# Optimization experiments

Measured on AMD Instinct MI355X. Metric: run time of the kernel, lower is better.

## Reference

```python
import jax, jax.numpy as jnp
import numpy as np

B, LQ, LK, H = 16, 8192, 128, 128  # note LK == H is required by the final matmul
SCALE = float(np.sqrt(H))


def setup_inputs() -> dict:
    key = jax.random.key(0)
    k1, k2, k3, k4, k5, k6 = jax.random.split(key, 6)
    x1 = jax.random.normal(k1, (B, LQ, H), dtype=jnp.float32)
    x2 = jax.random.normal(k2, (B, LK, H), dtype=jnp.float32)
    x3 = jax.random.randint(k3, (B, LQ, LK), 0, 2).astype(bool)
    bound = 1.0 / np.sqrt(H)  # torch Linear default init
    wq = jax.random.uniform(k4, (H, H), minval=-bound, maxval=bound, dtype=jnp.float32)
    wk = jax.random.uniform(k5, (H, H), minval=-bound, maxval=bound, dtype=jnp.float32)
    wv = jax.random.uniform(k6, (H, H), minval=-bound, maxval=bound, dtype=jnp.float32)
    return {"x1": x1, "x2": x2, "x3": x3, "wq": wq, "wk": wk, "wv": wv}


def reference(x1, x2, x3, wq, wk, wv):
    q = x1 @ wq.T                                   # (B, Lq, H)
    k = x2 @ wk.T                                   # (B, Lk, H)
    qk = jnp.einsum('bqh,bkh->bqk', q, k) / SCALE   # (B, Lq, Lk)
    qk = jnp.where(x3, -jnp.inf, qk)                # masked_fill_ where mask is True
    attn_weight = jax.nn.softmax(qk, axis=-1)       # softmax over Lk
    v = x2 @ wv.T                                   # (B, Lk, H)
    # v @ attn_weight^T: contracts v's H axis with attn_weight's Lk axis (H == Lk)
    attn = jnp.matmul(v, jnp.swapaxes(attn_weight, -2, -1))  # (B, Lk, Lq)
    return attn
```

## Files before the change

### kernel.cpp

```cpp
#include <hip/hip_runtime.h>
#include <hip/hip_bf16.h>
#include <stdint.h>

typedef __bf16 bf16_t;
typedef __bf16 bf16x8 __attribute__((ext_vector_type(8)));
typedef float  f32x4  __attribute__((ext_vector_type(4)));
typedef float  f32x16 __attribute__((ext_vector_type(16)));
typedef unsigned int uint;
typedef uint uintx4 __attribute__((ext_vector_type(4)));

#define MFMA16(a,b,c) __builtin_amdgcn_mfma_f32_16x16x32_bf16((a),(b),(c),0,0,0)
#define MFMA32(a,b,c) __builtin_amdgcn_mfma_f32_32x32x16_bf16((a),(b),(c),0,0,0)

constexpr int NB = 16;
constexpr int LQ = 8192;
constexpr int LK = 128;
constexpr int H  = 128;

constexpr float C1 = 1.4426950408889634f / 11.313708498984761f;

constexpr size_t WS_FLAG = 0;
constexpr size_t WS_MV   = 1024;

__device__ __forceinline__ unsigned swz(unsigned row, unsigned byte) {
  return row * 256u + (byte ^ ((row & 15u) << 4));
}

__device__ __forceinline__ bf16x8 cvt_frag(const float* p) {
  f32x4 u0 = *(const f32x4*)p;
  f32x4 u1 = *(const f32x4*)(p + 4);
  bf16x8 v;
  #pragma unroll
  for (int e = 0; e < 4; ++e) { v[e] = (bf16_t)u0[e]; v[e + 4] = (bf16_t)u1[e]; }
  return v;
}

__device__ __forceinline__ f32x16 zero16() {
  f32x16 z;
  #pragma unroll
  for (int i = 0; i < 16; ++i) z[i] = 0.f;
  return z;
}

__device__ __forceinline__ uint pkbf(float a, float b) {
  uint d;
  asm("v_cvt_pk_bf16_f32 %0, %1, %2" : "=v"(d) : "v"(a), "v"(b));
  return d;
}

__global__ __launch_bounds__(512) void prep_kernel(
    const float* __restrict__ x2, const float* __restrict__ wq,
    const float* __restrict__ wk, const float* __restrict__ wv,
    const unsigned* __restrict__ x3w, uint8_t* __restrict__ ws)
{
  __shared__ uint8_t sP[131072];
  __shared__ int sF32, sBig;
  const int tid = threadIdx.x;
  const int b = blockIdx.x >> 1, which = blockIdx.x & 1;
  const int l = tid & 63, w = tid >> 6, q31 = l & 31, hi2 = l >> 5;
  uint8_t* sOut = sP + 98304;

  if (which == 0) {
    if (blockIdx.x == 0) {
      if (tid == 0) { sF32 = 0; sBig = 0; }
      __syncthreads();
      int f = 0, g = 0;
      #pragma unroll
      for (int j = 0; j < 4; ++j) {
        unsigned v = x3w[tid * 4 + j];
        if (v == 0x3f800000u) f = 1;
        else if (v > 1u) g = 1;
      }
      if (f) sF32 = 1;
      if (g) sBig = 1;
      __syncthreads();
      if (tid == 0) *(int*)(ws + WS_FLAG) = (sF32 == 0 && sBig == 1) ? 1 : 0;
    }

    {
      const int row = tid >> 2, c0 = (tid & 3) * 32;
      #pragma unroll
      for (int wh = 0; wh < 2; ++wh) {
        const float* W = wh ? wk : wq;
        uint8_t* dst = sP + wh * 32768;
        const float* s = W + row * H + c0;
        #pragma unroll
        for (int j = 0; j < 32; ++j)
          *(bf16_t*)(dst + swz(c0 + j, row * 2)) = (bf16_t)s[j];
      }
    }
    __syncthreads();

    {
      const int lo = l & 15, hi = l >> 4;
      bf16x8 a4[4];
      #pragma unroll
      for (int kk = 0; kk < 4; ++kk)
        a4[kk] = *(const bf16x8*)(sP + swz(16 * w + lo, kk * 64 + hi * 16));
      bf16_t* W2T = (bf16_t*)(sP + 65536);
      #pragma unroll
      for (int t = 0; t < 8; ++t) {
        f32x4 c = {0.f, 0.f, 0.f, 0.f};
        #pragma unroll
        for (int kk = 0; kk < 4; ++kk)
          c = MFMA16(a4[kk], *(const bf16x8*)(sP + 32768 + swz(16 * t + lo, kk * 64 + hi * 16)), c);
        #pragma unroll
        for (int r = 0; r < 4; ++r)
          W2T[(16 * w + hi * 4 + r) * H + 16 * t + lo] = (bf16_t)c[r];
      }
    }
    __syncthreads();

    if (w < 4) {
      const int wb = w;
      bf16x8 axf[8];
      const float* x2r = x2 + ((size_t)b * LK + 32 * wb + q31) * H;
      #pragma unroll
      for (int kt = 0; kt < 8; ++kt)
        axf[kt] = cvt_frag(x2r + kt * 16 + 8 * hi2);
      const bf16_t* W2Tl = (const bf16_t*)(sP + 65536);
      #pragma unroll
      for (int nt = 0; nt < 4; ++nt) {
        f32x16 c = zero16();
        #pragma unroll
        for (int kt = 0; kt < 8; ++kt)
          c = MFMA32(axf[kt],
                     *(const bf16x8*)(W2Tl + (size_t)(nt * 32 + q31) * H + kt * 16 + 8 * hi2), c);
        #pragma unroll
        for (int r = 0; r < 16; ++r)
          *(bf16_t*)(sOut + swz(32 * wb + (r & 3) + 8 * (r >> 2) + 4 * hi2,
                                (nt * 32 + q31) * 2)) = (bf16_t)c[r];
      }
    }
  } else {
    if (w < 4) {
      const int wb = w;
      bf16x8 axf[8];
      const float* x2r = x2 + ((size_t)b * LK + 32 * wb + q31) * H;
      #pragma unroll
      for (int kt = 0; kt < 8; ++kt)
        axf[kt] = cvt_frag(x2r + kt * 16 + 8 * hi2);
      #pragma unroll
      for (int nt = 0; nt < 4; ++nt) {
        f32x16 c = zero16();
        #pragma unroll
        for (int kt = 0; kt < 8; ++kt)
          c = MFMA32(axf[kt],
                     cvt_frag(wv + (size_t)(nt * 32 + q31) * H + kt * 16 + 8 * hi2), c);
        #pragma unroll
        for (int r = 0; r < 16; ++r)
          *(bf16_t*)(sOut + swz(32 * wb + (r & 3) + 8 * (r >> 2) + 4 * hi2,
                                (nt * 32 + q31) * 2)) = (bf16_t)c[r];
      }
    }
  }
  __syncthreads();

  {
    const uint4* src = (const uint4*)sOut;
    uint4* dst = (uint4*)(ws + WS_MV + (size_t)b * 65536 + (size_t)which * 32768);
    #pragma unroll
    for (int j = 0; j < 4; ++j)
      dst[tid + j * 512] = src[tid + j * 512];
  }
}

__global__ __launch_bounds__(512, 4) void attn_kernel(
    const float* __restrict__ x1, const void* __restrict__ x3,
    const uint8_t* __restrict__ ws, float* __restrict__ out)
{
  __shared__ uint8_t sm[65536];
  uint8_t* sM = sm;
  uint8_t* sV = sm + 32768;

  const int tid = threadIdx.x, blk = blockIdx.x;
  const int b = blk >> 5, qc = (blk & 31) * 256;
  const int l = tid & 63, w = tid >> 6;
  const int q31 = l & 31, hi2 = l >> 5;
  const int byteMode = *(const int*)(ws + WS_FLAG);

  const int q0w = qc + w * 32;
  const size_t qrow = (size_t)b * LQ + q0w + q31;

  uint4 cp[8];
  {
    const uint4* mvsrc = (const uint4*)(ws + WS_MV + (size_t)b * 65536);
    #pragma unroll
    for (int j = 0; j < 8; ++j)
      cp[j] = mvsrc[tid + j * 512];
  }

  bf16x8 xbf[8];
  {
    const float* xr = x1 + qrow * H;
    #pragma unroll
    for (int kt = 0; kt < 8; ++kt)
      xbf[kt] = cvt_frag(xr + kt * 16 + 8 * hi2);
  }

  uint mu[16];
  if (byteMode) {
    const uint8_t* mp = (const uint8_t*)x3 + qrow * LK;
    #pragma unroll
    for (int jt = 0; jt < 4; ++jt)
      #pragma unroll
      for (int rg = 0; rg < 4; ++rg)
        mu[jt * 4 + rg] = *(const uint*)(mp + jt * 32 + 8 * rg + 4 * hi2);
  }

  {
    uint4* ldst = (uint4*)sm;
    #pragma unroll
    for (int j = 0; j < 8; ++j)
      ldst[tid + j * 512] = cp[j];
  }
  __syncthreads();

  const uint* mrowW = (const uint*)x3 + qrow * LK;
  bf16x8 pb[8];

  #pragma unroll
  for (int half = 0; half < 2; ++half) {
    const int jt0 = half * 2, jt1 = half * 2 + 1;
    f32x16 s0 = zero16(), s1 = zero16();
    #pragma unroll
    for (int kt = 0; kt < 8; ++kt) {
      s0 = MFMA32(*(const bf16x8*)(sM + swz(jt0 * 32 + q31, kt * 32 + hi2 * 16)),
                  xbf[kt], s0);
      s1 = MFMA32(*(const bf16x8*)(sM + swz(jt1 * 32 + q31, kt * 32 + hi2 * 16)),
                  xbf[kt], s1);
    }

    #pragma unroll
    for (int jj = 0; jj < 2; ++jj) {
      f32x16& sj = jj ? s1 : s0;
      const int jt = half * 2 + jj;
      #pragma unroll
      for (int rg = 0; rg < 4; ++rg) {
        uint m0, m1, m2, m3;
        if (byteMode) {
          uint u = mu[jt * 4 + rg];
          m0 = u & 0xffu; m1 = (u >> 8) & 0xffu; m2 = (u >> 16) & 0xffu; m3 = u >> 24;
        } else {
          uint4 mw = *(const uint4*)(mrowW + jt * 32 + 8 * rg + 4 * hi2);
          m0 = mw.x; m1 = mw.y; m2 = mw.z; m3 = mw.w;
        }
        float p0 = __builtin_amdgcn_exp2f(sj[rg * 4 + 0] * C1);
        float p1 = __builtin_amdgcn_exp2f(sj[rg * 4 + 1] * C1);
        float p2 = __builtin_amdgcn_exp2f(sj[rg * 4 + 2] * C1);
        float p3 = __builtin_amdgcn_exp2f(sj[rg * 4 + 3] * C1);
        sj[rg * 4 + 0] = m0 ? 0.f : p0;
        sj[rg * 4 + 1] = m1 ? 0.f : p1;
        sj[rg * 4 + 2] = m2 ? 0.f : p2;
        sj[rg * 4 + 3] = m3 ? 0.f : p3;
      }

      #pragma unroll
      for (int h = 0; h < 2; ++h) {
        uint A = pkbf(sj[h * 8 + 0], sj[h * 8 + 1]);
        uint C = pkbf(sj[h * 8 + 2], sj[h * 8 + 3]);
        uint B = pkbf(sj[h * 8 + 4], sj[h * 8 + 5]);
        uint D = pkbf(sj[h * 8 + 6], sj[h * 8 + 7]);
        asm("v_permlane32_swap_b32 %0, %1" : "+v"(A), "+v"(B));
        asm("v_permlane32_swap_b32 %0, %1" : "+v"(C), "+v"(D));
        uintx4 t; t.x = A; t.y = C; t.z = B; t.w = D;
        pb[jt * 2 + h] = __builtin_bit_cast(bf16x8, t);
      }
    }
  }

  bf16x8 ones1;
  #pragma unroll
  for (int e = 0; e < 8; ++e) ones1[e] = (bf16_t)1.f;

  f32x16 dacc = zero16();
  {
    f32x16 o0 = zero16(), o1 = zero16();
    #pragma unroll
    for (int kt = 0; kt < 8; ++kt) {
      dacc = MFMA32(ones1, pb[kt], dacc);
      o0 = MFMA32(*(const bf16x8*)(sV + swz(0 * 32 + q31, kt * 32 + hi2 * 16)), pb[kt], o0);
      o1 = MFMA32(*(const bf16x8*)(sV + swz(1 * 32 + q31, kt * 32 + hi2 * 16)), pb[kt], o1);
    }
    const float inv = 1.0f / dacc[0];
    #pragma unroll
    for (int r = 0; r < 16; ++r) {
      const int ibase = (r & 3) + 8 * (r >> 2) + 4 * hi2;
      out[((size_t)b * LK + ibase) * LQ + q0w + q31] = o0[r] * inv;
      out[((size_t)b * LK + 32 + ibase) * LQ + q0w + q31] = o1[r] * inv;
    }
  }

  {
    const float inv = 1.0f / dacc[0];
    f32x16 o2 = zero16(), o3 = zero16();
    #pragma unroll
    for (int kt = 0; kt < 8; ++kt) {
      o2 = MFMA32(*(const bf16x8*)(sV + swz(2 * 32 + q31, kt * 32 + hi2 * 16)), pb[kt], o2);
      o3 = MFMA32(*(const bf16x8*)(sV + swz(3 * 32 + q31, kt * 32 + hi2 * 16)), pb[kt], o3);
    }
    #pragma unroll
    for (int r = 0; r < 16; ++r) {
      const int ibase = (r & 3) + 8 * (r >> 2) + 4 * hi2;
      out[((size_t)b * LK + 64 + ibase) * LQ + q0w + q31] = o2[r] * inv;
      out[((size_t)b * LK + 96 + ibase) * LQ + q0w + q31] = o3[r] * inv;
    }
  }
}

extern "C" void kernel_launch(void* const* d_in, const int* in_sizes, int n_in,
                              void* d_out, int out_size, void* d_ws, size_t ws_size,
                              hipStream_t stream) {
  const float* x1 = (const float*)d_in[0];
  const float* x2 = (const float*)d_in[1];
  const void*  x3 = d_in[2];
  const float* wq = (const float*)d_in[3];
  const float* wk = (const float*)d_in[4];
  const float* wv = (const float*)d_in[5];
  uint8_t* ws = (uint8_t*)d_ws;
  float* out = (float*)d_out;

  prep_kernel<<<2 * NB, 512, 0, stream>>>(x2, wq, wk, wv, (const unsigned*)x3, ws);
  attn_kernel<<<NB * (LQ / 256), 512, 0, stream>>>(x1, x3, ws, out);
}
```

Baseline: 49.75 us.

## Process two query tiles per wave with prefetch overlap and async LDS loads

Result: faster. 47.40 us (-4.7%).

```diff
diff --git a/kernel.cpp b/kernel.cpp
--- a/kernel.cpp
+++ b/kernel.cpp
@@ -46,6 +46,12 @@
   uint d;
   asm("v_cvt_pk_bf16_f32 %0, %1, %2" : "=v"(d) : "v"(a), "v"(b));
   return d;
+}
+
+__device__ __forceinline__ void gl16(const void* g, void* l) {
+  __builtin_amdgcn_global_load_lds(
+      (const __attribute__((address_space(1))) uint32_t*)g,
+      (__attribute__((address_space(3))) uint32_t*)l, 16, 0, 0);
 }
 
 __global__ __launch_bounds__(512) void prep_kernel(
@@ -165,7 +171,113 @@
   }
 }
 
-__global__ __launch_bounds__(512, 4) void attn_kernel(
+
+#define CONV_S_PB(XR, MU, QROW)                                                \
+  {                                                                            \
+    bf16x8 xbf[8];                                                             \
+    _Pragma("unroll")                                                          \
+    for (int kt = 0; kt < 8; ++kt) {                                           \
+      _Pragma("unroll")                                                        \
+      for (int e = 0; e < 4; ++e) {                                            \
+        xbf[kt][e]     = (bf16_t)XR[2 * kt][e];                                \
+        xbf[kt][e + 4] = (bf16_t)XR[2 * kt + 1][e];                            \
+      }                                                                        \
+    }                                                                          \
+    const uint* mrowW = (const uint*)x3 + (QROW) * LK;                         \
+    _Pragma("unroll")                                                          \
+    for (int half = 0; half < 2; ++half) {                                     \
+      const int jt0 = half * 2, jt1 = half * 2 + 1;                            \
+      f32x16 s0 = zero16(), s1 = zero16();                                     \
+      __builtin_amdgcn_s_setprio(1);                                           \
+      _Pragma("unroll")                                                        \
+      for (int kt = 0; kt < 8; ++kt) {                                         \
+        s0 = MFMA32(*(const bf16x8*)(sM + swz(jt0 * 32 + q31, kt * 32 + hi2 * 16)), \
+                    xbf[kt], s0);                                              \
+        s1 = MFMA32(*(const bf16x8*)(sM + swz(jt1 * 32 + q31, kt * 32 + hi2 * 16)), \
+                    xbf[kt], s1);                                              \
+      }                                                                        \
+      __builtin_amdgcn_s_setprio(0);                                           \
+      _Pragma("unroll")                                                        \
+      for (int jj = 0; jj < 2; ++jj) {                                         \
+        f32x16& sj = jj ? s1 : s0;                                             \
+        const int jt = half * 2 + jj;                                          \
+        _Pragma("unroll")                                                      \
+        for (int rg = 0; rg < 4; ++rg) {                                       \
+          uint m0, m1, m2, m3;                                                 \
+          if (byteMode) {                                                      \
+            uint u = MU[jt * 4 + rg];                                          \
+            m0 = u & 0xffu; m1 = (u >> 8) & 0xffu;                             \
+            m2 = (u >> 16) & 0xffu; m3 = u >> 24;                              \
+          } else {                                                             \
+            uint4 mw = *(const uint4*)(mrowW + jt * 32 + 8 * rg + 4 * hi2);    \
+            m0 = mw.x; m1 = mw.y; m2 = mw.z; m3 = mw.w;                        \
+          }                                                                    \
+          float p0 = __builtin_amdgcn_exp2f(sj[rg * 4 + 0] * C1);              \
+          float p1 = __builtin_amdgcn_exp2f(sj[rg * 4 + 1] * C1);              \
+          float p2 = __builtin_amdgcn_exp2f(sj[rg * 4 + 2] * C1);              \
+          float p3 = __builtin_amdgcn_exp2f(sj[rg * 4 + 3] * C1);              \
+          sj[rg * 4 + 0] = m0 ? 0.f : p0;                                      \
+          sj[rg * 4 + 1] = m1 ? 0.f : p1;                                      \
+          sj[rg * 4 + 2] = m2 ? 0.f : p2;                                      \
+          sj[rg * 4 + 3] = m3 ? 0.f : p3;                                      \
+        }                                                                      \
+        _Pragma("unroll")                                                      \
+        for (int h = 0; h < 2; ++h) {                                          \
+          uint A = pkbf(sj[h * 8 + 0], sj[h * 8 + 1]);                         \
+          uint C = pkbf(sj[h * 8 + 2], sj[h * 8 + 3]);                         \
+          uint B = pkbf(sj[h * 8 + 4], sj[h * 8 + 5]);                         \
+          uint D = pkbf(sj[h * 8 + 6], sj[h * 8 + 7]);                         \
+          asm("v_permlane32_swap_b32 %0, %1" : "+v"(A), "+v"(B));              \
+          asm("v_permlane32_swap_b32 %0, %1" : "+v"(C), "+v"(D));              \
+          uintx4 t2; t2.x = A; t2.y = C; t2.z = B; t2.w = D;                   \
+          pb[jt * 2 + h] = __builtin_bit_cast(bf16x8, t2);                     \
+        }                                                                      \
+      }                                                                        \
+    }                                                                          \
+  }
+
+#define O_STORE(Q0W)                                                           \
+  {                                                                            \
+    f32x16 dacc = zero16();                                                    \
+    {                                                                          \
+      f32x16 o0 = zero16(), o1 = zero16();                                     \
+      __builtin_amdgcn_s_setprio(1);                                           \
+      _Pragma("unroll")                                                        \
+      for (int kt = 0; kt < 8; ++kt) {                                         \
+        dacc = MFMA32(ones1, pb[kt], dacc);                                    \
+        o0 = MFMA32(*(const bf16x8*)(sV + swz(0 * 32 + q31, kt * 32 + hi2 * 16)), pb[kt], o0); \
+        o1 = MFMA32(*(const bf16x8*)(sV + swz(1 * 32 + q31, kt * 32 + hi2 * 16)), pb[kt], o1); \
+      }                                                                        \
+      __builtin_amdgcn_s_setprio(0);                                           \
+      const float inv = 1.0f / dacc[0];                                        \
+      _Pragma("unroll")                                                        \
+      for (int r = 0; r < 16; ++r) {                                           \
+        const int ibase = (r & 3) + 8 * (r >> 2) + 4 * hi2;                    \
+        __builtin_nontemporal_store(o0[r] * inv,                               \
+            &out[((size_t)b * LK + ibase) * LQ + (Q0W) + q31]);                \
+        __builtin_nontemporal_store(o1[r] * inv,                               \
+            &out[((size_t)b * LK + 32 + ibase) * LQ + (Q0W) + q31]);           \
+      }                                                                        \
+      f32x16 o2 = zero16(), o3 = zero16();                                     \
+      __builtin_amdgcn_s_setprio(1);                                           \
+      _Pragma("unroll")                                                        \
+      for (int kt = 0; kt < 8; ++kt) {                                         \
+        o2 = MFMA32(*(const bf16x8*)(sV + swz(2 * 32 + q31, kt * 32 + hi2 * 16)), pb[kt], o2); \
+        o3 = MFMA32(*(const bf16x8*)(sV + swz(3 * 32 + q31, kt * 32 + hi2 * 16)), pb[kt], o3); \
+      }                                                                        \
+      __builtin_amdgcn_s_setprio(0);                                           \
+      _Pragma("unroll")                                                        \
+      for (int r = 0; r < 16; ++r) {                                           \
+        const int ibase = (r & 3) + 8 * (r >> 2) + 4 * hi2;                    \
+        __builtin_nontemporal_store(o2[r] * inv,                               \
+            &out[((size_t)b * LK + 64 + ibase) * LQ + (Q0W) + q31]);           \
+        __builtin_nontemporal_store(o3[r] * inv,                               \
+            &out[((size_t)b * LK + 96 + ibase) * LQ + (Q0W) + q31]);           \
+      }                                                                        \
+    }                                                                          \
+  }
+
+__global__ __launch_bounds__(256, 2) void attn_kernel(
     const float* __restrict__ x1, const void* __restrict__ x3,
     const uint8_t* __restrict__ ws, float* __restrict__ out)
 {
@@ -174,138 +286,77 @@
   uint8_t* sV = sm + 32768;
 
   const int tid = threadIdx.x, blk = blockIdx.x;
-  const int b = blk >> 5, qc = (blk & 31) * 256;
-  const int l = tid & 63, w = tid >> 6;
+  const int xcd = blk & 7;
+  const int t   = blk >> 3;
+  const int b   = ((t & 1) << 3) | xcd;
+  const int qc  = (t >> 1) * 256;
+  const int l = tid & 63, w4 = tid >> 6;
   const int q31 = l & 31, hi2 = l >> 5;
   const int byteMode = *(const int*)(ws + WS_FLAG);
 
-  const int q0w = qc + w * 32;
-  const size_t qrow = (size_t)b * LQ + q0w + q31;
-
-  uint4 cp[8];
+  const int q0w0 = qc + w4 * 64;
+  const int q0w1 = q0w0 + 32;
+  const size_t qrow0 = (size_t)b * LQ + q0w0 + q31;
+  const size_t qrow1 = qrow0 + 32;
+
   {
-    const uint4* mvsrc = (const uint4*)(ws + WS_MV + (size_t)b * 65536);
+    const uint8_t* g = ws + WS_MV + (size_t)b * 65536;
     #pragma unroll
-    for (int j = 0; j < 8; ++j)
-      cp[j] = mvsrc[tid + j * 512];
-  }
-
-  bf16x8 xbf[8];
+    for (int j = 0; j < 16; ++j)
+      gl16(g + tid * 16 + j * 4096, sm + tid * 16 + j * 4096);
+  }
+
+  f32x4 xr0[16];
+  uint mu0[16];
   {
-    const float* xr = x1 + qrow * H;
-    #pragma unroll
-    for (int kt = 0; kt < 8; ++kt)
-      xbf[kt] = cvt_frag(xr + kt * 16 + 8 * hi2);
-  }
-
-  uint mu[16];
-  if (byteMode) {
-    const uint8_t* mp = (const uint8_t*)x3 + qrow * LK;
-    #pragma unroll
-    for (int jt = 0; jt < 4; ++jt)
-      #pragma unroll
-      for (int rg = 0; rg < 4; ++rg)
-        mu[jt * 4 + rg] = *(const uint*)(mp + jt * 32 + 8 * rg + 4 * hi2);
-  }
-
-  {
-    uint4* ldst = (uint4*)sm;
-    #pragma unroll
-    for (int j = 0; j < 8; ++j)
-      ldst[tid + j * 512] = cp[j];
-  }
-  __syncthreads();
-
-  const uint* mrowW = (const uint*)x3 + qrow * LK;
-  bf16x8 pb[8];
-
-  #pragma unroll
-  for (int half = 0; half < 2; ++half) {
-    const int jt0 = half * 2, jt1 = half * 2 + 1;
-    f32x16 s0 = zero16(), s1 = zero16();
+    const float* xp = x1 + qrow0 * H;
     #pragma unroll
     for (int kt = 0; kt < 8; ++kt) {
-      s0 = MFMA32(*(const bf16x8*)(sM + swz(jt0 * 32 + q31, kt * 32 + hi2 * 16)),
-                  xbf[kt], s0);
-      s1 = MFMA32(*(const bf16x8*)(sM + swz(jt1 * 32 + q31, kt * 32 + hi2 * 16)),
-                  xbf[kt], s1);
-    }
-
-    #pragma unroll
-    for (int jj = 0; jj < 2; ++jj) {
-      f32x16& sj = jj ? s1 : s0;
-      const int jt = half * 2 + jj;
-      #pragma unroll
-      for (int rg = 0; rg < 4; ++rg) {
-        uint m0, m1, m2, m3;
-        if (byteMode) {
-          uint u = mu[jt * 4 + rg];
-          m0 = u & 0xffu; m1 = (u >> 8) & 0xffu; m2 = (u >> 16) & 0xffu; m3 = u >> 24;
-        } else {
-          uint4 mw = *(const uint4*)(mrowW + jt * 32 + 8 * rg + 4 * hi2);
-          m0 = mw.x; m1 = mw.y; m2 = mw.z; m3 = mw.w;
-        }
-        float p0 = __builtin_amdgcn_exp2f(sj[rg * 4 + 0] * C1);
-        float p1 = __builtin_amdgcn_exp2f(sj[rg * 4 + 1] * C1);
-        float p2 = __builtin_amdgcn_exp2f(sj[rg * 4 + 2] * C1);
-        float p3 = __builtin_amdgcn_exp2f(sj[rg * 4 + 3] * C1);
-        sj[rg * 4 + 0] = m0 ? 0.f : p0;
-        sj[rg * 4 + 1] = m1 ? 0.f : p1;
-        sj[rg * 4 + 2] = m2 ? 0.f : p2;
-        sj[rg * 4 + 3] = m3 ? 0.f : p3;
-      }
-
-      #pragma unroll
-      for (int h = 0; h < 2; ++h) {
-        uint A = pkbf(sj[h * 8 + 0], sj[h * 8 + 1]);
-        uint C = pkbf(sj[h * 8 + 2], sj[h * 8 + 3]);
-        uint B = pkbf(sj[h * 8 + 4], sj[h * 8 + 5]);
-        uint D = pkbf(sj[h * 8 + 6], sj[h * 8 + 7]);
-        asm("v_permlane32_swap_b32 %0, %1" : "+v"(A), "+v"(B));
-        asm("v_permlane32_swap_b32 %0, %1" : "+v"(C), "+v"(D));
-        uintx4 t; t.x = A; t.y = C; t.z = B; t.w = D;
-        pb[jt * 2 + h] = __builtin_bit_cast(bf16x8, t);
-      }
-    }
-  }
+      xr0[2 * kt]     = *(const f32x4*)(xp + kt * 16 + 8 * hi2);
+      xr0[2 * kt + 1] = *(const f32x4*)(xp + kt * 16 + 8 * hi2 + 4);
+    }
+    if (byteMode) {
+      const uint8_t* mp = (const uint8_t*)x3 + qrow0 * LK;
+      #pragma unroll
+      for (int jt = 0; jt < 4; ++jt)
+        #pragma unroll
+        for (int rg = 0; rg < 4; ++rg)
+          mu0[jt * 4 + rg] = *(const uint*)(mp + jt * 32 + 8 * rg + 4 * hi2);
+    }
+  }
+  __syncthreads();
 
   bf16x8 ones1;
   #pragma unroll
   for (int e = 0; e < 8; ++e) ones1[e] = (bf16_t)1.f;
 
-  f32x16 dacc = zero16();
+  bf16x8 pb[8];
+
+  CONV_S_PB(xr0, mu0, qrow0)
+
+  f32x4 xr1[16];
+  uint mu1[16];
   {
-    f32x16 o0 = zero16(), o1 = zero16();
+    const float* xp = x1 + qrow1 * H;
     #pragma unroll
     for (int kt = 0; kt < 8; ++kt) {
-      dacc = MFMA32(ones1, pb[kt], dacc);
-      o0 = MFMA32(*(const bf16x8*)(sV + swz(0 * 32 + q31, kt * 32 + hi2 * 16)), pb[kt], o0);
-      o1 = MFMA32(*(const bf16x8*)(sV + swz(1 * 32 + q31, kt * 32 + hi2 * 16)), pb[kt], o1);
-    }
-    const float inv = 1.0f / dacc[0];
-    #pragma unroll
-    for (int r = 0; r < 16; ++r) {
-      const int ibase = (r & 3) + 8 * (r >> 2) + 4 * hi2;
-      out[((size_t)b * LK + ibase) * LQ + q0w + q31] = o0[r] * inv;
-      out[((size_t)b * LK + 32 + ibase) * LQ + q0w + q31] = o1[r] * inv;
-    }
-  }
-
-  {
-    const float inv = 1.0f / dacc[0];
-    f32x16 o2 = zero16(), o3 = zero16();
-    #pragma unroll
-    for (int kt = 0; kt < 8; ++kt) {
-      o2 = MFMA32(*(const bf16x8*)(sV + swz(2 * 32 + q31, kt * 32 + hi2 * 16)), pb[kt], o2);
-      o3 = MFMA32(*(const bf16x8*)(sV + swz(3 * 32 + q31, kt * 32 + hi2 * 16)), pb[kt], o3);
-    }
-    #pragma unroll
-    for (int r = 0; r < 16; ++r) {
-      const int ibase = (r & 3) + 8 * (r >> 2) + 4 * hi2;
-      out[((size_t)b * LK + 64 + ibase) * LQ + q0w + q31] = o2[r] * inv;
-      out[((size_t)b * LK + 96 + ibase) * LQ + q0w + q31] = o3[r] * inv;
-    }
-  }
+      xr1[2 * kt]     = *(const f32x4*)(xp + kt * 16 + 8 * hi2);
+      xr1[2 * kt + 1] = *(const f32x4*)(xp + kt * 16 + 8 * hi2 + 4);
+    }
+    if (byteMode) {
+      const uint8_t* mp = (const uint8_t*)x3 + qrow1 * LK;
+      #pragma unroll
+      for (int jt = 0; jt < 4; ++jt)
+        #pragma unroll
+        for (int rg = 0; rg < 4; ++rg)
+          mu1[jt * 4 + rg] = *(const uint*)(mp + jt * 32 + 8 * rg + 4 * hi2);
+    }
+  }
+
+  O_STORE(q0w0)
+
+  CONV_S_PB(xr1, mu1, qrow1)
+  O_STORE(q0w1)
 }
 
 extern "C" void kernel_launch(void* const* d_in, const int* in_sizes, int n_in,
@@ -321,5 +372,5 @@
   float* out = (float*)d_out;
 
   prep_kernel<<<2 * NB, 512, 0, stream>>>(x2, wq, wk, wv, (const unsigned*)x3, ws);
-  attn_kernel<<<NB * (LQ / 256), 512, 0, stream>>>(x1, x3, ws, out);
-}
+  attn_kernel<<<NB * (LQ / 256), 256, 0, stream>>>(x1, x3, ws, out);
+}
```
